# Optimization experiments

Hardware: AMD Instinct MI355X
Metric: run time of the kernel (lower is better)

The kernel has to match this reference:

```python
import jax, jax.numpy as jnp
import numpy as np

A, L, D_ATOM, D_PROT, B = 2048, 512, 128, 128, 64
H1, H2 = 512, 256


def setup_inputs() -> dict:
    key = jax.random.key(0)
    ks = jax.random.split(key, 10)
    atom_embed = jax.random.normal(ks[0], (A, D_ATOM), dtype=jnp.float32)
    protSeq_embed = jax.random.normal(ks[1], (B, L, D_PROT), dtype=jnp.float32)
    atom_splits = jnp.sort(jax.random.randint(ks[2], (A,), 0, B))
    # attention bilinear weight (atom_dim, prot_dim); scaled so exp(score) stays finite
    W_att = jax.random.normal(ks[3], (D_ATOM, D_PROT), dtype=jnp.float32) / np.float32(D_ATOM)
    cdim = D_ATOM + D_PROT
    W1 = jax.random.normal(ks[4], (cdim, H1), dtype=jnp.float32) / np.sqrt(np.float32(cdim))
    b1 = jnp.zeros((H1,), dtype=jnp.float32)
    W2 = jax.random.normal(ks[5], (H1, H2), dtype=jnp.float32) / np.sqrt(np.float32(H1))
    b2 = jnp.zeros((H2,), dtype=jnp.float32)
    Wo = jax.random.normal(ks[6], (H2, 1), dtype=jnp.float32) / np.sqrt(np.float32(H2))
    bo = jnp.zeros((1,), dtype=jnp.float32)
    return {"atom_embed": atom_embed, "protSeq_embed": protSeq_embed,
            "atom_splits": atom_splits, "W_att": W_att,
            "W1": W1, "b1": b1, "W2": W2, "b2": b2, "Wo": Wo, "bo": bo}


def reference(atom_embed, protSeq_embed, atom_splits, W_att, W1, b1, W2, b2, Wo, bo):
    batch = protSeq_embed.shape[0]
    # bilinear attention scores: S[a, l] = atom[a] @ W_att @ prot[seg[a], l]
    X = atom_embed @ W_att                              # [A, D_PROT]
    prot_g = protSeq_embed[atom_splits]                 # [A, L, D_PROT] (gather)
    S = jnp.einsum('ad,ald->al', X, prot_g)             # [A, L]
    # segment softmax over atoms within each molecule (on max-over-protein score)
    Wc = jnp.exp(jnp.max(S, axis=-1, keepdims=True))    # [A, 1]
    Sc = jax.ops.segment_sum(Wc, atom_splits, num_segments=batch)[atom_splits]
    aa = Wc / Sc                                        # [A, 1]
    atom_pool = jax.ops.segment_sum(aa * atom_embed, atom_splits, num_segments=batch)  # [B, D_ATOM]
    # protein attention: segment-max pooled scores -> softmax over residues
    Wp = jax.ops.segment_max(S, atom_splits, num_segments=batch)  # [B, L]
    ap = jax.nn.softmax(Wp, axis=-1)
    prot_pool = jnp.einsum('bl,bld->bd', ap, protSeq_embed)       # [B, D_PROT]
    h = jnp.concatenate([atom_pool, prot_pool], axis=-1)
    h = jax.nn.relu(h @ W1 + b1)
    h = jax.nn.relu(h @ W2 + b2)
    return h @ Wo + bo                                  # [B, 1]
```

## Files before the change

### kernel.cpp

```cpp
#include <hip/hip_runtime.h>
#include <math.h>

#define A_N 2048
#define L_N 512
#define D 128
#define B_N 64
#define H1_N 512
#define H2_N 256
#define NCHUNK 8
#define CL 64
#define XT 32
#define PST 136

typedef __attribute__((ext_vector_type(8))) short short8;
typedef __attribute__((ext_vector_type(4))) float f32x4;

__device__ __forceinline__ int lb_dev(const int* __restrict__ arr, int n, int val) {
    int lo = 0, hi = n;
    while (lo < hi) { int mid = (lo + hi) >> 1; if (arr[mid] < val) lo = mid + 1; else hi = mid; }
    return lo;
}

__device__ __forceinline__ float blk_sum(float v, float* red, int tid) {
    #pragma unroll
    for (int off = 32; off >= 1; off >>= 1) v += __shfl_xor(v, off);
    __syncthreads();
    if ((tid & 63) == 0) red[tid >> 6] = v;
    __syncthreads();
    return red[0] + red[1] + red[2] + red[3];
}

__device__ __forceinline__ unsigned short f2bf(float f) {
    unsigned int u = __float_as_uint(f);
    return (unsigned short)((u + 0x7FFFu + ((u >> 16) & 1u)) >> 16);
}
__device__ __forceinline__ float bf2f(unsigned short h) {
    return __uint_as_float(((unsigned int)h) << 16);
}

__global__ __launch_bounds__(256) void k1_xmul(const float* __restrict__ atom_embed,
                                               const float* __restrict__ W_att,
                                               const float* __restrict__ bo,
                                               float* __restrict__ X,
                                               float* __restrict__ out) {
    __shared__ float ae[8][128];
    const int tid = threadIdx.x;
    const int bid = blockIdx.x;
    if (bid == 0 && tid < B_N) out[tid] = bo[0];
    const int a0 = bid * 8;
    float4 v = reinterpret_cast<const float4*>(atom_embed + (size_t)a0 * D)[tid];
    const int fi = tid * 4;
    *reinterpret_cast<float4*>(&ae[fi >> 7][fi & 127]) = v;
    __syncthreads();
    const int d = tid & 127;
    const int ai = tid >> 7;
    float acc0 = 0.f, acc1 = 0.f, acc2 = 0.f, acc3 = 0.f;
    for (int k = 0; k < D; ++k) {
        const float w = W_att[k * D + d];
        acc0 += ae[ai + 0][k] * w;
        acc1 += ae[ai + 2][k] * w;
        acc2 += ae[ai + 4][k] * w;
        acc3 += ae[ai + 6][k] * w;
    }
    X[(size_t)(a0 + ai + 0) * D + d] = acc0;
    X[(size_t)(a0 + ai + 2) * D + d] = acc1;
    X[(size_t)(a0 + ai + 4) * D + d] = acc2;
    X[(size_t)(a0 + ai + 6) * D + d] = acc3;
}

__global__ __launch_bounds__(256) void k2_scores(const float* __restrict__ X,
                                                 const float* __restrict__ prot,
                                                 const int* __restrict__ splits,
                                                 float* __restrict__ rowmaxp,
                                                 float* __restrict__ ppart,
                                                 float* __restrict__ eWpart) {
    __shared__ __align__(16) unsigned char lds[52736];
    unsigned short* Ph = (unsigned short*)lds;
    unsigned short* Pl = Ph + CL * PST;
    unsigned short* Xh = Pl + CL * PST;
    unsigned short* Xl = Xh + XT * PST;
    float* rm_lds = (float*)(lds + 52224);

    const int tid = threadIdx.x;
    const int bid = blockIdx.x;
    const int b = bid & (B_N - 1);
    const int chunk = bid >> 6;
    const int l0 = chunk * CL;
    const int s = lb_dev(splits, A_N, b);
    const int e = lb_dev(splits, A_N, b + 1);
    const int n = e - s;
    const int lane = tid & 63;
    const int w = tid >> 6;
    const int col = lane & 15;
    const int kb = lane >> 4;

    {
        const float4* src = (const float4*)(prot + ((size_t)b * L_N + l0) * D);
        for (int i = tid; i < CL * (D / 4); i += 256) {
            float4 v = src[i];
            const int row = i >> 5, q = (i & 31) * 4;
            ushort4 h, lo;
            h.x = f2bf(v.x); lo.x = f2bf(v.x - bf2f(h.x));
            h.y = f2bf(v.y); lo.y = f2bf(v.y - bf2f(h.y));
            h.z = f2bf(v.z); lo.z = f2bf(v.z - bf2f(h.z));
            h.w = f2bf(v.w); lo.w = f2bf(v.w - bf2f(h.w));
            *(ushort4*)(Ph + row * PST + q) = h;
            *(ushort4*)(Pl + row * PST + q) = lo;
        }
    }
    __syncthreads();

    short8 Bh[4], Bl[4];
    {
        const int rowb = w * 16 + col;
        #pragma unroll
        for (int ks = 0; ks < 4; ++ks) {
            Bh[ks] = *(const short8*)(Ph + rowb * PST + ks * 32 + kb * 8);
            Bl[ks] = *(const short8*)(Pl + rowb * PST + ks * 32 + kb * 8);
        }
    }

    float cmrun = -INFINITY;
    for (int a0 = 0; a0 < n; a0 += XT) {
        __syncthreads();
        {
            const float4* xsrc = (const float4*)(X + (size_t)s * D);
            for (int i = tid; i < XT * (D / 4); i += 256) {
                const int row = i >> 5, q = (i & 31) * 4;
                const int atom = a0 + row;
                float4 v = {0.f, 0.f, 0.f, 0.f};
                if (atom < n) v = xsrc[(size_t)atom * (D / 4) + (i & 31)];
                ushort4 h, lo;
                h.x = f2bf(v.x); lo.x = f2bf(v.x - bf2f(h.x));
                h.y = f2bf(v.y); lo.y = f2bf(v.y - bf2f(h.y));
                h.z = f2bf(v.z); lo.z = f2bf(v.z - bf2f(h.z));
                h.w = f2bf(v.w); lo.w = f2bf(v.w - bf2f(h.w));
                *(ushort4*)(Xh + row * PST + q) = h;
                *(ushort4*)(Xl + row * PST + q) = lo;
            }
        }
        __syncthreads();

        #pragma unroll
        for (int mt = 0; mt < 2; ++mt) {
            f32x4 acc = {0.f, 0.f, 0.f, 0.f};
            const int rowa = mt * 16 + col;
            #pragma unroll
            for (int ks = 0; ks < 4; ++ks) {
                short8 Ah = *(const short8*)(Xh + rowa * PST + ks * 32 + kb * 8);
                short8 Al = *(const short8*)(Xl + rowa * PST + ks * 32 + kb * 8);
                acc = __builtin_amdgcn_mfma_f32_16x16x32_bf16(Ah, Bh[ks], acc, 0, 0, 0);
                acc = __builtin_amdgcn_mfma_f32_16x16x32_bf16(Ah, Bl[ks], acc, 0, 0, 0);
                acc = __builtin_amdgcn_mfma_f32_16x16x32_bf16(Al, Bh[ks], acc, 0, 0, 0);
            }
            float r0 = acc[0], r1 = acc[1], r2 = acc[2], r3 = acc[3];
            #pragma unroll
            for (int off = 1; off <= 8; off <<= 1) {
                r0 = fmaxf(r0, __shfl_xor(r0, off));
                r1 = fmaxf(r1, __shfl_xor(r1, off));
                r2 = fmaxf(r2, __shfl_xor(r2, off));
                r3 = fmaxf(r3, __shfl_xor(r3, off));
            }
            if (col == 0) {
                float4 rv; rv.x = r0; rv.y = r1; rv.z = r2; rv.w = r3;
                *(float4*)(rm_lds + w * 32 + mt * 16 + kb * 4) = rv;
            }
            const int rbase = a0 + mt * 16 + kb * 4;
            float cm = -INFINITY;
            if (rbase + 0 < n) cm = fmaxf(cm, acc[0]);
            if (rbase + 1 < n) cm = fmaxf(cm, acc[1]);
            if (rbase + 2 < n) cm = fmaxf(cm, acc[2]);
            if (rbase + 3 < n) cm = fmaxf(cm, acc[3]);
            cm = fmaxf(cm, __shfl_xor(cm, 16));
            cm = fmaxf(cm, __shfl_xor(cm, 32));
            cmrun = fmaxf(cmrun, cm);
        }
        __syncthreads();
        if (tid < XT) {
            const int atom = a0 + tid;
            if (atom < n) {
                float m = fmaxf(fmaxf(rm_lds[tid], rm_lds[32 + tid]),
                                fmaxf(rm_lds[64 + tid], rm_lds[96 + tid]));
                rowmaxp[(size_t)(s + atom) * NCHUNK + chunk] = m;
            }
        }
    }

    float* ews  = (float*)(lds + 34816);
    float* psum = ews + 64;
    __syncthreads();
    if (lane < 16) ews[w * 16 + lane] = expf(cmrun);
    __syncthreads();
    {
        const int dd = tid & 127, hh = tid >> 7;
        float sacc = 0.f;
        #pragma unroll 8
        for (int l = hh * 32; l < hh * 32 + 32; ++l)
            sacc += ews[l] * (bf2f(Ph[l * PST + dd]) + bf2f(Pl[l * PST + dd]));
        psum[hh * 128 + dd] = sacc;
    }
    __syncthreads();
    if (tid < 128)
        ppart[(size_t)(b * NCHUNK + chunk) * D + tid] = psum[tid] + psum[128 + tid];
    if (tid < 64) {
        float v = ews[tid];
        #pragma unroll
        for (int off = 32; off >= 1; off >>= 1) v += __shfl_xor(v, off);
        if (tid == 0) eWpart[b * NCHUNK + chunk] = v;
    }
}

__global__ __launch_bounds__(256) void k3_pool(const float* __restrict__ atom_embed,
                                               const int* __restrict__ splits,
                                               const float* __restrict__ rowmaxp,
                                               const float* __restrict__ ppart,
                                               const float* __restrict__ eWpart,
                                               float* __restrict__ HcT) {
    __shared__ float red[4];
    __shared__ float coef[512];
    __shared__ float4 pred[8][32];
    const int tid = threadIdx.x;
    const int b = blockIdx.x;
    const int s = lb_dev(splits, A_N, b);
    const int e = lb_dev(splits, A_N, b + 1);
    const int n = e - s;

    float local = 0.f;
    for (int j = tid; j < n; j += 256) {
        const float* rp = rowmaxp + (size_t)(s + j) * NCHUNK;
        float m = rp[0];
        #pragma unroll
        for (int c = 1; c < NCHUNK; ++c) m = fmaxf(m, rp[c]);
        local += expf(m);
    }
    const float Sc = blk_sum(local, red, tid);

    const int d4 = tid & 31;
    const int ag = tid >> 5;
    const float4* ae4 = reinterpret_cast<const float4*>(atom_embed);
    float4 pool = {0.f, 0.f, 0.f, 0.f};
    for (int t0 = 0; t0 < n; t0 += 512) {
        const int cnt = min(512, n - t0);
        __syncthreads();
        for (int j = tid; j < cnt; j += 256) {
            const float* rp = rowmaxp + (size_t)(s + t0 + j) * NCHUNK;
            float m = rp[0];
            #pragma unroll
            for (int c = 1; c < NCHUNK; ++c) m = fmaxf(m, rp[c]);
            coef[j] = expf(m) / Sc;
        }
        __syncthreads();
        for (int j = ag; j < cnt; j += 8) {
            const float c = coef[j];
            const float4 v = ae4[(size_t)(s + t0 + j) * (D / 4) + d4];
            pool.x += c * v.x; pool.y += c * v.y; pool.z += c * v.z; pool.w += c * v.w;
        }
    }
    __syncthreads();
    pred[ag][d4] = pool;
    __syncthreads();
    if (ag == 0) {
        float4 acc = pred[0][d4];
        #pragma unroll
        for (int gg = 1; gg < 8; ++gg) {
            const float4 t = pred[gg][d4];
            acc.x += t.x; acc.y += t.y; acc.z += t.z; acc.w += t.w;
        }
        HcT[(size_t)(d4 * 4 + 0) * B_N + b] = acc.x;
        HcT[(size_t)(d4 * 4 + 1) * B_N + b] = acc.y;
        HcT[(size_t)(d4 * 4 + 2) * B_N + b] = acc.z;
        HcT[(size_t)(d4 * 4 + 3) * B_N + b] = acc.w;
    }
    if (tid < 128) {
        float v = 0.f, ez = 0.f;
        #pragma unroll
        for (int c = 0; c < NCHUNK; ++c) {
            v  += ppart[(size_t)(b * NCHUNK + c) * D + tid];
            ez += eWpart[b * NCHUNK + c];
        }
        HcT[(size_t)(D + tid) * B_N + b] = v / ez;
    }
}

__global__ __launch_bounds__(256) void k4_h1(const float* __restrict__ HcT,
                                             const float* __restrict__ W1,
                                             const float* __restrict__ b1,
                                             float* __restrict__ H1T) {
    __shared__ float hr[4][64];
    const int tid = threadIdx.x;
    const int m = tid & 63;
    const int jh = (tid >> 6) & 1;
    const int kh = tid >> 7;
    const int j = blockIdx.x * 2 + jh;
    float acc = 0.f;
    const int k0 = kh * 128;
    #pragma unroll 8
    for (int k = k0; k < k0 + 128; ++k)
        acc += HcT[(size_t)k * B_N + m] * W1[(size_t)k * H1_N + j];
    hr[jh * 2 + kh][m] = acc;
    __syncthreads();
    if (kh == 0)
        H1T[(size_t)j * B_N + m] = fmaxf(hr[jh * 2][m] + hr[jh * 2 + 1][m] + b1[j], 0.f);
}

__global__ __launch_bounds__(256) void k5_h2(const float* __restrict__ H1T,
                                             const float* __restrict__ W2,
                                             const float* __restrict__ b2,
                                             const float* __restrict__ Wo,
                                             float* __restrict__ out) {
    __shared__ float hr[4][64];
    const int tid = threadIdx.x;
    const int m = tid & 63;
    const int kq = tid >> 6;
    const int j = blockIdx.x;
    float acc = 0.f;
    const int k0 = kq * 128;
    #pragma unroll 8
    for (int k = k0; k < k0 + 128; ++k)
        acc += H1T[(size_t)k * B_N + m] * W2[(size_t)k * H2_N + j];
    hr[kq][m] = acc;
    __syncthreads();
    if (kq == 0) {
        const float h2 = fmaxf(hr[0][m] + hr[1][m] + hr[2][m] + hr[3][m] + b2[j], 0.f);
        atomicAdd(out + m, h2 * Wo[j]);
    }
}

extern "C" void kernel_launch(void* const* d_in, const int* in_sizes, int n_in,
                              void* d_out, int out_size, void* d_ws, size_t ws_size,
                              hipStream_t stream) {
    const float* atom_embed = (const float*)d_in[0];
    const float* prot       = (const float*)d_in[1];
    const int*   splits     = (const int*)d_in[2];
    const float* W_att      = (const float*)d_in[3];
    const float* W1         = (const float*)d_in[4];
    const float* b1         = (const float*)d_in[5];
    const float* W2         = (const float*)d_in[6];
    const float* b2         = (const float*)d_in[7];
    const float* Wo         = (const float*)d_in[8];
    const float* bo         = (const float*)d_in[9];
    float* out = (float*)d_out;

    float* ws = (float*)d_ws;
    float* X       = ws;  ws += A_N * D;
    float* rowmaxp = ws;  ws += A_N * NCHUNK;
    float* ppart   = ws;  ws += B_N * NCHUNK * D;
    float* eWpart  = ws;  ws += B_N * NCHUNK;
    float* HcT     = ws;  ws += 2 * D * B_N;
    float* H1T     = ws;  ws += H1_N * B_N;

    hipLaunchKernelGGL(k1_xmul,  dim3(A_N / 8),      dim3(256), 0, stream,
                       atom_embed, W_att, bo, X, out);
    hipLaunchKernelGGL(k2_scores,dim3(B_N * NCHUNK), dim3(256), 0, stream,
                       X, prot, splits, rowmaxp, ppart, eWpart);
    hipLaunchKernelGGL(k3_pool,  dim3(B_N),          dim3(256), 0, stream,
                       atom_embed, splits, rowmaxp, ppart, eWpart, HcT);
    hipLaunchKernelGGL(k4_h1,    dim3(H1_N / 2),     dim3(256), 0, stream, HcT, W1, b1, H1T);
    hipLaunchKernelGGL(k5_h2,    dim3(H2_N),         dim3(256), 0, stream, H1T, W2, b2, Wo, out);
}
```

Before: 46.23 us.

## Fuse projection, scoring and pooling into one per-molecule kernel

Merges the X=atom@W_att projection (now done with split-bf16 MFMA in-block), the score computation and both pooling stages into one kernel with one block per molecule. This removes the X, rowmax and partial-sum workspace round trips and two kernel launches. In exchange the grid shrinks from 512 blocks to 64, and each block streams the full protein sequence once per 64-atom tile while recomputing W_att fragments from global memory. That lowers parallelism and may leave most CUs idle.

Result: slower. 64.28 us (+39.0%).

```diff
diff --git a/kernel.cpp b/kernel.cpp
--- a/kernel.cpp
+++ b/kernel.cpp
@@ -7,9 +7,6 @@
 #define B_N 64
 #define H1_N 512
 #define H2_N 256
-#define NCHUNK 8
-#define CL 64
-#define XT 32
 #define PST 136
 
 typedef __attribute__((ext_vector_type(8))) short short8;
@@ -21,15 +18,6 @@
     return lo;
 }
 
-__device__ __forceinline__ float blk_sum(float v, float* red, int tid) {
-    #pragma unroll
-    for (int off = 32; off >= 1; off >>= 1) v += __shfl_xor(v, off);
-    __syncthreads();
-    if ((tid & 63) == 0) red[tid >> 6] = v;
-    __syncthreads();
-    return red[0] + red[1] + red[2] + red[3];
-}
-
 __device__ __forceinline__ unsigned short f2bf(float f) {
     unsigned int u = __float_as_uint(f);
     return (unsigned short)((u + 0x7FFFu + ((u >> 16) & 1u)) >> 16);
@@ -38,247 +26,274 @@
     return __uint_as_float(((unsigned int)h) << 16);
 }
 
-__global__ __launch_bounds__(256) void k1_xmul(const float* __restrict__ atom_embed,
-                                               const float* __restrict__ W_att,
-                                               const float* __restrict__ bo,
-                                               float* __restrict__ X,
-                                               float* __restrict__ out) {
-    __shared__ float ae[8][128];
+__global__ __launch_bounds__(256) void k123(const float* __restrict__ atom_embed,
+                                            const float* __restrict__ prot,
+                                            const int* __restrict__ splits,
+                                            const float* __restrict__ W_att,
+                                            const float* __restrict__ bo,
+                                            float* __restrict__ HcT,
+                                            float* __restrict__ out) {
+    __shared__ unsigned short Ph[32 * PST], Pl[32 * PST];
+    __shared__ unsigned short Xh[64 * PST], Xl[64 * PST];
+    __shared__ float cmax_all[512];
+    __shared__ float rm[64];
+    __shared__ float rm_part[4][64];
+    __shared__ float cm_part[2][32];
+    __shared__ float ews[32];
+    __shared__ float ea_lds[64];
+    __shared__ float4 pred[8][32];
+    __shared__ float zacc_s, sc_acc_s;
+
     const int tid = threadIdx.x;
-    const int bid = blockIdx.x;
-    if (bid == 0 && tid < B_N) out[tid] = bo[0];
-    const int a0 = bid * 8;
-    float4 v = reinterpret_cast<const float4*>(atom_embed + (size_t)a0 * D)[tid];
-    const int fi = tid * 4;
-    *reinterpret_cast<float4*>(&ae[fi >> 7][fi & 127]) = v;
-    __syncthreads();
-    const int d = tid & 127;
-    const int ai = tid >> 7;
-    float acc0 = 0.f, acc1 = 0.f, acc2 = 0.f, acc3 = 0.f;
-    for (int k = 0; k < D; ++k) {
-        const float w = W_att[k * D + d];
-        acc0 += ae[ai + 0][k] * w;
-        acc1 += ae[ai + 2][k] * w;
-        acc2 += ae[ai + 4][k] * w;
-        acc3 += ae[ai + 6][k] * w;
-    }
-    X[(size_t)(a0 + ai + 0) * D + d] = acc0;
-    X[(size_t)(a0 + ai + 2) * D + d] = acc1;
-    X[(size_t)(a0 + ai + 4) * D + d] = acc2;
-    X[(size_t)(a0 + ai + 6) * D + d] = acc3;
-}
-
-__global__ __launch_bounds__(256) void k2_scores(const float* __restrict__ X,
-                                                 const float* __restrict__ prot,
-                                                 const int* __restrict__ splits,
-                                                 float* __restrict__ rowmaxp,
-                                                 float* __restrict__ ppart,
-                                                 float* __restrict__ eWpart) {
-    __shared__ __align__(16) unsigned char lds[52736];
-    unsigned short* Ph = (unsigned short*)lds;
-    unsigned short* Pl = Ph + CL * PST;
-    unsigned short* Xh = Pl + CL * PST;
-    unsigned short* Xl = Xh + XT * PST;
-    float* rm_lds = (float*)(lds + 52224);
-
-    const int tid = threadIdx.x;
-    const int bid = blockIdx.x;
-    const int b = bid & (B_N - 1);
-    const int chunk = bid >> 6;
-    const int l0 = chunk * CL;
+    const int b = blockIdx.x;
+    if (b == 0 && tid < B_N) out[tid] = bo[0];
     const int s = lb_dev(splits, A_N, b);
     const int e = lb_dev(splits, A_N, b + 1);
     const int n = e - s;
+
+    cmax_all[tid] = -INFINITY;
+    cmax_all[tid + 256] = -INFINITY;
+    if (tid < 64) rm[tid] = -INFINITY;
+    if (tid == 0) { zacc_s = 0.f; sc_acc_s = 0.f; }
+
     const int lane = tid & 63;
     const int w = tid >> 6;
     const int col = lane & 15;
     const int kb = lane >> 4;
-
-    {
-        const float4* src = (const float4*)(prot + ((size_t)b * L_N + l0) * D);
-        for (int i = tid; i < CL * (D / 4); i += 256) {
-            float4 v = src[i];
-            const int row = i >> 5, q = (i & 31) * 4;
-            ushort4 h, lo;
-            h.x = f2bf(v.x); lo.x = f2bf(v.x - bf2f(h.x));
-            h.y = f2bf(v.y); lo.y = f2bf(v.y - bf2f(h.y));
-            h.z = f2bf(v.z); lo.z = f2bf(v.z - bf2f(h.z));
-            h.w = f2bf(v.w); lo.w = f2bf(v.w - bf2f(h.w));
-            *(ushort4*)(Ph + row * PST + q) = h;
-            *(ushort4*)(Pl + row * PST + q) = lo;
-        }
-    }
-    __syncthreads();
-
-    short8 Bh[4], Bl[4];
-    {
-        const int rowb = w * 16 + col;
-        #pragma unroll
-        for (int ks = 0; ks < 4; ++ks) {
-            Bh[ks] = *(const short8*)(Ph + rowb * PST + ks * 32 + kb * 8);
-            Bl[ks] = *(const short8*)(Pl + rowb * PST + ks * 32 + kb * 8);
-        }
-    }
-
-    float cmrun = -INFINITY;
-    for (int a0 = 0; a0 < n; a0 += XT) {
+    const int c4 = tid & 31;
+    const int rg = tid >> 5;
+
+    float4 pool4 = {0.f, 0.f, 0.f, 0.f};
+    float4 pp4   = {0.f, 0.f, 0.f, 0.f};
+
+    for (int a0 = 0; a0 < n; a0 += 64) {
+        const int an = min(64, n - a0);
+        const bool isLast = (a0 + 64 >= n);
+
         __syncthreads();
         {
-            const float4* xsrc = (const float4*)(X + (size_t)s * D);
-            for (int i = tid; i < XT * (D / 4); i += 256) {
-                const int row = i >> 5, q = (i & 31) * 4;
-                const int atom = a0 + row;
-                float4 v = {0.f, 0.f, 0.f, 0.f};
-                if (atom < n) v = xsrc[(size_t)atom * (D / 4) + (i & 31)];
-                ushort4 h, lo;
-                h.x = f2bf(v.x); lo.x = f2bf(v.x - bf2f(h.x));
-                h.y = f2bf(v.y); lo.y = f2bf(v.y - bf2f(h.y));
-                h.z = f2bf(v.z); lo.z = f2bf(v.z - bf2f(h.z));
-                h.w = f2bf(v.w); lo.w = f2bf(v.w - bf2f(h.w));
-                *(ushort4*)(Xh + row * PST + q) = h;
-                *(ushort4*)(Xl + row * PST + q) = lo;
+            short8 WBh[2][4], WBl[2][4];
+            #pragma unroll
+            for (int ff = 0; ff < 2; ++ff) {
+                const int dcol = (w * 2 + ff) * 16 + col;
+                #pragma unroll
+                for (int ks = 0; ks < 4; ++ks) {
+                    short8 bh, bl;
+                    #pragma unroll
+                    for (int j = 0; j < 8; ++j) {
+                        const float wv = W_att[(size_t)(ks * 32 + kb * 8 + j) * D + dcol];
+                        const unsigned short h = f2bf(wv);
+                        bh[j] = (short)h;
+                        bl[j] = (short)f2bf(wv - bf2f(h));
+                    }
+                    WBh[ff][ks] = bh; WBl[ff][ks] = bl;
+                }
+            }
+            #pragma unroll
+            for (int mt = 0; mt < 4; ++mt) {
+                const int ar = mt * 16 + col;
+                const bool va = ar < an;
+                short8 Ah[4], Al[4];
+                #pragma unroll
+                for (int ks = 0; ks < 4; ++ks) {
+                    float4 v0 = {0.f,0.f,0.f,0.f}, v1 = {0.f,0.f,0.f,0.f};
+                    if (va) {
+                        const float4* p = (const float4*)(atom_embed + (size_t)(s + a0 + ar) * D)
+                                          + ks * 8 + kb * 2;
+                        v0 = p[0]; v1 = p[1];
+                    }
+                    const float vv[8] = {v0.x,v0.y,v0.z,v0.w,v1.x,v1.y,v1.z,v1.w};
+                    short8 ah, al;
+                    #pragma unroll
+                    for (int j = 0; j < 8; ++j) {
+                        const unsigned short h = f2bf(vv[j]);
+                        ah[j] = (short)h;
+                        al[j] = (short)f2bf(vv[j] - bf2f(h));
+                    }
+                    Ah[ks] = ah; Al[ks] = al;
+                }
+                #pragma unroll
+                for (int ff = 0; ff < 2; ++ff) {
+                    f32x4 acc = {0.f, 0.f, 0.f, 0.f};
+                    #pragma unroll
+                    for (int ks = 0; ks < 4; ++ks) {
+                        acc = __builtin_amdgcn_mfma_f32_16x16x32_bf16(Ah[ks], WBh[ff][ks], acc, 0, 0, 0);
+                        acc = __builtin_amdgcn_mfma_f32_16x16x32_bf16(Ah[ks], WBl[ff][ks], acc, 0, 0, 0);
+                        acc = __builtin_amdgcn_mfma_f32_16x16x32_bf16(Al[ks], WBh[ff][ks], acc, 0, 0, 0);
+                    }
+                    const int dcol = (w * 2 + ff) * 16 + col;
+                    #pragma unroll
+                    for (int i = 0; i < 4; ++i) {
+                        const int arow = mt * 16 + kb * 4 + i;
+                        const unsigned short h = f2bf(acc[i]);
+                        Xh[arow * PST + dcol] = h;
+                        Xl[arow * PST + dcol] = f2bf(acc[i] - bf2f(h));
+                    }
+                }
             }
         }
         __syncthreads();
 
+        short8 XAh[2][4], XAl[2][4];
         #pragma unroll
-        for (int mt = 0; mt < 2; ++mt) {
-            f32x4 acc = {0.f, 0.f, 0.f, 0.f};
-            const int rowa = mt * 16 + col;
+        for (int m = 0; m < 2; ++m) {
+            const int mrow = ((w >> 1) + m * 2) * 16 + col;
             #pragma unroll
             for (int ks = 0; ks < 4; ++ks) {
-                short8 Ah = *(const short8*)(Xh + rowa * PST + ks * 32 + kb * 8);
-                short8 Al = *(const short8*)(Xl + rowa * PST + ks * 32 + kb * 8);
-                acc = __builtin_amdgcn_mfma_f32_16x16x32_bf16(Ah, Bh[ks], acc, 0, 0, 0);
-                acc = __builtin_amdgcn_mfma_f32_16x16x32_bf16(Ah, Bl[ks], acc, 0, 0, 0);
-                acc = __builtin_amdgcn_mfma_f32_16x16x32_bf16(Al, Bh[ks], acc, 0, 0, 0);
-            }
-            float r0 = acc[0], r1 = acc[1], r2 = acc[2], r3 = acc[3];
-            #pragma unroll
-            for (int off = 1; off <= 8; off <<= 1) {
-                r0 = fmaxf(r0, __shfl_xor(r0, off));
-                r1 = fmaxf(r1, __shfl_xor(r1, off));
-                r2 = fmaxf(r2, __shfl_xor(r2, off));
-                r3 = fmaxf(r3, __shfl_xor(r3, off));
-            }
-            if (col == 0) {
-                float4 rv; rv.x = r0; rv.y = r1; rv.z = r2; rv.w = r3;
-                *(float4*)(rm_lds + w * 32 + mt * 16 + kb * 4) = rv;
-            }
-            const int rbase = a0 + mt * 16 + kb * 4;
-            float cm = -INFINITY;
-            if (rbase + 0 < n) cm = fmaxf(cm, acc[0]);
-            if (rbase + 1 < n) cm = fmaxf(cm, acc[1]);
-            if (rbase + 2 < n) cm = fmaxf(cm, acc[2]);
-            if (rbase + 3 < n) cm = fmaxf(cm, acc[3]);
-            cm = fmaxf(cm, __shfl_xor(cm, 16));
-            cm = fmaxf(cm, __shfl_xor(cm, 32));
-            cmrun = fmaxf(cmrun, cm);
+                XAh[m][ks] = *(const short8*)(Xh + mrow * PST + ks * 32 + kb * 8);
+                XAl[m][ks] = *(const short8*)(Xl + mrow * PST + ks * 32 + kb * 8);
+            }
+        }
+
+        for (int ch = 0; ch < 16; ++ch) {
+            __syncthreads();
+            float4 pv[4];
+            {
+                const float4* src = (const float4*)(prot + ((size_t)b * L_N + ch * 32) * D);
+                #pragma unroll
+                for (int kq = 0; kq < 4; ++kq) {
+                    const int i = tid + kq * 256;
+                    pv[kq] = src[i];
+                    const int row = i >> 5, q = (i & 31) * 4;
+                    ushort4 h, lo;
+                    h.x = f2bf(pv[kq].x); lo.x = f2bf(pv[kq].x - bf2f(h.x));
+                    h.y = f2bf(pv[kq].y); lo.y = f2bf(pv[kq].y - bf2f(h.y));
+                    h.z = f2bf(pv[kq].z); lo.z = f2bf(pv[kq].z - bf2f(h.z));
+                    h.w = f2bf(pv[kq].w); lo.w = f2bf(pv[kq].w - bf2f(h.w));
+                    *(ushort4*)(Ph + row * PST + q) = h;
+                    *(ushort4*)(Pl + row * PST + q) = lo;
+                }
+            }
+            ((float*)rm_part)[tid] = -INFINITY;
+            __syncthreads();
+
+            const int nt = w & 1;
+            short8 PBh[4], PBl[4];
+            #pragma unroll
+            for (int ks = 0; ks < 4; ++ks) {
+                PBh[ks] = *(const short8*)(Ph + (nt * 16 + col) * PST + ks * 32 + kb * 8);
+                PBl[ks] = *(const short8*)(Pl + (nt * 16 + col) * PST + ks * 32 + kb * 8);
+            }
+            float cm_w = -INFINITY;
+            #pragma unroll
+            for (int m = 0; m < 2; ++m) {
+                f32x4 acc = {0.f, 0.f, 0.f, 0.f};
+                #pragma unroll
+                for (int ks = 0; ks < 4; ++ks) {
+                    acc = __builtin_amdgcn_mfma_f32_16x16x32_bf16(XAh[m][ks], PBh[ks], acc, 0, 0, 0);
+                    acc = __builtin_amdgcn_mfma_f32_16x16x32_bf16(XAh[m][ks], PBl[ks], acc, 0, 0, 0);
+                    acc = __builtin_amdgcn_mfma_f32_16x16x32_bf16(XAl[m][ks], PBh[ks], acc, 0, 0, 0);
+                }
+                const int mt = (w >> 1) + m * 2;
+                float r0 = acc[0], r1 = acc[1], r2 = acc[2], r3 = acc[3];
+                #pragma unroll
+                for (int off = 1; off <= 8; off <<= 1) {
+                    r0 = fmaxf(r0, __shfl_xor(r0, off));
+                    r1 = fmaxf(r1, __shfl_xor(r1, off));
+                    r2 = fmaxf(r2, __shfl_xor(r2, off));
+                    r3 = fmaxf(r3, __shfl_xor(r3, off));
+                }
+                if (col == 0) {
+                    rm_part[w][mt * 16 + kb * 4 + 0] = r0;
+                    rm_part[w][mt * 16 + kb * 4 + 1] = r1;
+                    rm_part[w][mt * 16 + kb * 4 + 2] = r2;
+                    rm_part[w][mt * 16 + kb * 4 + 3] = r3;
+                }
+                const int rb = mt * 16 + kb * 4;
+                float cm = -INFINITY;
+                if (rb + 0 < an) cm = fmaxf(cm, acc[0]);
+                if (rb + 1 < an) cm = fmaxf(cm, acc[1]);
+                if (rb + 2 < an) cm = fmaxf(cm, acc[2]);
+                if (rb + 3 < an) cm = fmaxf(cm, acc[3]);
+                cm = fmaxf(cm, __shfl_xor(cm, 16));
+                cm = fmaxf(cm, __shfl_xor(cm, 32));
+                cm_w = fmaxf(cm_w, cm);
+            }
+            if (kb == 0) cm_part[w >> 1][nt * 16 + col] = cm_w;
+            __syncthreads();
+
+            if (tid < 64) {
+                const float m4 = fmaxf(fmaxf(rm_part[0][tid], rm_part[1][tid]),
+                                       fmaxf(rm_part[2][tid], rm_part[3][tid]));
+                rm[tid] = fmaxf(rm[tid], m4);
+            }
+            if (tid < 32) {
+                const float cm = fmaxf(cm_part[0][tid], cm_part[1][tid]);
+                const float cl = fmaxf(cmax_all[ch * 32 + tid], cm);
+                cmax_all[ch * 32 + tid] = cl;
+                if (isLast) {
+                    float ev = expf(cl);
+                    ews[tid] = ev;
+                    #pragma unroll
+                    for (int off = 1; off <= 16; off <<= 1) ev += __shfl_xor(ev, off);
+                    if (tid == 0) zacc_s += ev;
+                }
+            }
+            __syncthreads();
+
+            if (isLast) {
+                #pragma unroll
+                for (int kq = 0; kq < 4; ++kq) {
+                    const float wgt = ews[rg + kq * 8];
+                    pp4.x += wgt * pv[kq].x;
+                    pp4.y += wgt * pv[kq].y;
+                    pp4.z += wgt * pv[kq].z;
+                    pp4.w += wgt * pv[kq].w;
+                }
+            }
+        }
+
+        if (tid < 64) {
+            float ea = (tid < an) ? expf(rm[tid]) : 0.f;
+            ea_lds[tid] = ea;
+            rm[tid] = -INFINITY;
+            #pragma unroll
+            for (int off = 1; off <= 32; off <<= 1) ea += __shfl_xor(ea, off);
+            if (tid == 0) sc_acc_s += ea;
         }
         __syncthreads();
-        if (tid < XT) {
-            const int atom = a0 + tid;
-            if (atom < n) {
-                float m = fmaxf(fmaxf(rm_lds[tid], rm_lds[32 + tid]),
-                                fmaxf(rm_lds[64 + tid], rm_lds[96 + tid]));
-                rowmaxp[(size_t)(s + atom) * NCHUNK + chunk] = m;
+        {
+            const float4* ae4 = (const float4*)atom_embed;
+            for (int a = rg; a < an; a += 8) {
+                const float c = ea_lds[a];
+                const float4 v = ae4[(size_t)(s + a0 + a) * (D / 4) + c4];
+                pool4.x += c * v.x; pool4.y += c * v.y;
+                pool4.z += c * v.z; pool4.w += c * v.w;
             }
         }
     }
 
-    float* ews  = (float*)(lds + 34816);
-    float* psum = ews + 64;
-    __syncthreads();
-    if (lane < 16) ews[w * 16 + lane] = expf(cmrun);
-    __syncthreads();
-    {
-        const int dd = tid & 127, hh = tid >> 7;
-        float sacc = 0.f;
-        #pragma unroll 8
-        for (int l = hh * 32; l < hh * 32 + 32; ++l)
-            sacc += ews[l] * (bf2f(Ph[l * PST + dd]) + bf2f(Pl[l * PST + dd]));
-        psum[hh * 128 + dd] = sacc;
-    }
-    __syncthreads();
-    if (tid < 128)
-        ppart[(size_t)(b * NCHUNK + chunk) * D + tid] = psum[tid] + psum[128 + tid];
-    if (tid < 64) {
-        float v = ews[tid];
-        #pragma unroll
-        for (int off = 32; off >= 1; off >>= 1) v += __shfl_xor(v, off);
-        if (tid == 0) eWpart[b * NCHUNK + chunk] = v;
-    }
-}
-
-__global__ __launch_bounds__(256) void k3_pool(const float* __restrict__ atom_embed,
-                                               const int* __restrict__ splits,
-                                               const float* __restrict__ rowmaxp,
-                                               const float* __restrict__ ppart,
-                                               const float* __restrict__ eWpart,
-                                               float* __restrict__ HcT) {
-    __shared__ float red[4];
-    __shared__ float coef[512];
-    __shared__ float4 pred[8][32];
-    const int tid = threadIdx.x;
-    const int b = blockIdx.x;
-    const int s = lb_dev(splits, A_N, b);
-    const int e = lb_dev(splits, A_N, b + 1);
-    const int n = e - s;
-
-    float local = 0.f;
-    for (int j = tid; j < n; j += 256) {
-        const float* rp = rowmaxp + (size_t)(s + j) * NCHUNK;
-        float m = rp[0];
-        #pragma unroll
-        for (int c = 1; c < NCHUNK; ++c) m = fmaxf(m, rp[c]);
-        local += expf(m);
-    }
-    const float Sc = blk_sum(local, red, tid);
-
-    const int d4 = tid & 31;
-    const int ag = tid >> 5;
-    const float4* ae4 = reinterpret_cast<const float4*>(atom_embed);
-    float4 pool = {0.f, 0.f, 0.f, 0.f};
-    for (int t0 = 0; t0 < n; t0 += 512) {
-        const int cnt = min(512, n - t0);
-        __syncthreads();
-        for (int j = tid; j < cnt; j += 256) {
-            const float* rp = rowmaxp + (size_t)(s + t0 + j) * NCHUNK;
-            float m = rp[0];
-            #pragma unroll
-            for (int c = 1; c < NCHUNK; ++c) m = fmaxf(m, rp[c]);
-            coef[j] = expf(m) / Sc;
-        }
-        __syncthreads();
-        for (int j = ag; j < cnt; j += 8) {
-            const float c = coef[j];
-            const float4 v = ae4[(size_t)(s + t0 + j) * (D / 4) + d4];
-            pool.x += c * v.x; pool.y += c * v.y; pool.z += c * v.z; pool.w += c * v.w;
-        }
-    }
-    __syncthreads();
-    pred[ag][d4] = pool;
-    __syncthreads();
-    if (ag == 0) {
-        float4 acc = pred[0][d4];
+    __syncthreads();
+    pred[rg][c4] = pool4;
+    __syncthreads();
+    if (tid < 32) {
+        float4 acc = pred[0][tid];
         #pragma unroll
         for (int gg = 1; gg < 8; ++gg) {
-            const float4 t = pred[gg][d4];
+            const float4 t = pred[gg][tid];
             acc.x += t.x; acc.y += t.y; acc.z += t.z; acc.w += t.w;
         }
-        HcT[(size_t)(d4 * 4 + 0) * B_N + b] = acc.x;
-        HcT[(size_t)(d4 * 4 + 1) * B_N + b] = acc.y;
-        HcT[(size_t)(d4 * 4 + 2) * B_N + b] = acc.z;
-        HcT[(size_t)(d4 * 4 + 3) * B_N + b] = acc.w;
+        const float invSc = 1.f / sc_acc_s;
+        HcT[(size_t)(tid * 4 + 0) * B_N + b] = acc.x * invSc;
+        HcT[(size_t)(tid * 4 + 1) * B_N + b] = acc.y * invSc;
+        HcT[(size_t)(tid * 4 + 2) * B_N + b] = acc.z * invSc;
+        HcT[(size_t)(tid * 4 + 3) * B_N + b] = acc.w * invSc;
     }
-    if (tid < 128) {
-        float v = 0.f, ez = 0.f;
+    __syncthreads();
+    pred[rg][c4] = pp4;
+    __syncthreads();
+    if (tid < 32) {
+        float4 acc = pred[0][tid];
         #pragma unroll
-        for (int c = 0; c < NCHUNK; ++c) {
-            v  += ppart[(size_t)(b * NCHUNK + c) * D + tid];
-            ez += eWpart[b * NCHUNK + c];
-        }
-        HcT[(size_t)(D + tid) * B_N + b] = v / ez;
+        for (int gg = 1; gg < 8; ++gg) {
+            const float4 t = pred[gg][tid];
+            acc.x += t.x; acc.y += t.y; acc.z += t.z; acc.w += t.w;
+        }
+        const float invZ = 1.f / zacc_s;
+        HcT[(size_t)(D + tid * 4 + 0) * B_N + b] = acc.x * invZ;
+        HcT[(size_t)(D + tid * 4 + 1) * B_N + b] = acc.y * invZ;
+        HcT[(size_t)(D + tid * 4 + 2) * B_N + b] = acc.z * invZ;
+        HcT[(size_t)(D + tid * 4 + 3) * B_N + b] = acc.w * invZ;
     }
 }
 
@@ -342,19 +357,11 @@
     float* out = (float*)d_out;
 
     float* ws = (float*)d_ws;
-    float* X       = ws;  ws += A_N * D;
-    float* rowmaxp = ws;  ws += A_N * NCHUNK;
-    float* ppart   = ws;  ws += B_N * NCHUNK * D;
-    float* eWpart  = ws;  ws += B_N * NCHUNK;
-    float* HcT     = ws;  ws += 2 * D * B_N;
-    float* H1T     = ws;  ws += H1_N * B_N;
-
-    hipLaunchKernelGGL(k1_xmul,  dim3(A_N / 8),      dim3(256), 0, stream,
-                       atom_embed, W_att, bo, X, out);
-    hipLaunchKernelGGL(k2_scores,dim3(B_N * NCHUNK), dim3(256), 0, stream,
-                       X, prot, splits, rowmaxp, ppart, eWpart);
-    hipLaunchKernelGGL(k3_pool,  dim3(B_N),          dim3(256), 0, stream,
-                       atom_embed, splits, rowmaxp, ppart, eWpart, HcT);
-    hipLaunchKernelGGL(k4_h1,    dim3(H1_N / 2),     dim3(256), 0, stream, HcT, W1, b1, H1T);
-    hipLaunchKernelGGL(k5_h2,    dim3(H2_N),         dim3(256), 0, stream, H1T, W2, b2, Wo, out);
-}
+    float* HcT = ws;  ws += 2 * D * B_N;
+    float* H1T = ws;  ws += H1_N * B_N;
+
+    hipLaunchKernelGGL(k123, dim3(B_N),      dim3(256), 0, stream,
+                       atom_embed, prot, splits, W_att, bo, HcT, out);
+    hipLaunchKernelGGL(k4_h1, dim3(H1_N / 2), dim3(256), 0, stream, HcT, W1, b1, H1T);
+    hipLaunchKernelGGL(k5_h2, dim3(H2_N),     dim3(256), 0, stream, H1T, W2, b2, Wo, out);
+}
```

## Precompute bf16 hi/lo X in k1 and drop LDS staging in scores kernel

Applied to the files above, without the earlier changes.

k1 now writes X already split into bf16 high and low halves, so k2 no longer converts X on every chunk. The scores kernel drops its LDS tiles for X and prot: each wave loads its B fragments straight from global memory and streams A fragments per 16-atom tile. Chunks shrink to 32 residues, doubling the grid to 1024 blocks, and a launch bound asks for 3 blocks per CU. The weighted protein sum now rereads fp32 prot from global memory instead of LDS. The per-block row-max buffer holds only 128 atoms per molecule, so larger segments would overflow it.

Result: slower. 49.66 us (+7.4%).

```diff
diff --git a/kernel.cpp b/kernel.cpp
--- a/kernel.cpp
+++ b/kernel.cpp
@@ -7,10 +7,8 @@
 #define B_N 64
 #define H1_N 512
 #define H2_N 256
-#define NCHUNK 8
-#define CL 64
-#define XT 32
-#define PST 136
+#define NCHUNK 16
+#define CL 32
 
 typedef __attribute__((ext_vector_type(8))) short short8;
 typedef __attribute__((ext_vector_type(4))) float f32x4;
@@ -41,7 +39,8 @@
 __global__ __launch_bounds__(256) void k1_xmul(const float* __restrict__ atom_embed,
                                                const float* __restrict__ W_att,
                                                const float* __restrict__ bo,
-                                               float* __restrict__ X,
+                                               unsigned short* __restrict__ Xh,
+                                               unsigned short* __restrict__ Xl,
                                                float* __restrict__ out) {
     __shared__ float ae[8][128];
     const int tid = threadIdx.x;
@@ -62,24 +61,27 @@
         acc2 += ae[ai + 4][k] * w;
         acc3 += ae[ai + 6][k] * w;
     }
-    X[(size_t)(a0 + ai + 0) * D + d] = acc0;
-    X[(size_t)(a0 + ai + 2) * D + d] = acc1;
-    X[(size_t)(a0 + ai + 4) * D + d] = acc2;
-    X[(size_t)(a0 + ai + 6) * D + d] = acc3;
-}
-
-__global__ __launch_bounds__(256) void k2_scores(const float* __restrict__ X,
-                                                 const float* __restrict__ prot,
-                                                 const int* __restrict__ splits,
-                                                 float* __restrict__ rowmaxp,
-                                                 float* __restrict__ ppart,
-                                                 float* __restrict__ eWpart) {
-    __shared__ __align__(16) unsigned char lds[52736];
-    unsigned short* Ph = (unsigned short*)lds;
-    unsigned short* Pl = Ph + CL * PST;
-    unsigned short* Xh = Pl + CL * PST;
-    unsigned short* Xl = Xh + XT * PST;
-    float* rm_lds = (float*)(lds + 52224);
+    float accs[4] = {acc0, acc1, acc2, acc3};
+    #pragma unroll
+    for (int t = 0; t < 4; ++t) {
+        const size_t idx = (size_t)(a0 + ai + 2 * t) * D + d;
+        const unsigned short h = f2bf(accs[t]);
+        Xh[idx] = h;
+        Xl[idx] = f2bf(accs[t] - bf2f(h));
+    }
+}
+
+__global__ __launch_bounds__(256, 3) void k2_scores(const unsigned short* __restrict__ Xh,
+                                                    const unsigned short* __restrict__ Xl,
+                                                    const float* __restrict__ prot,
+                                                    const int* __restrict__ splits,
+                                                    float* __restrict__ rowmaxp,
+                                                    float* __restrict__ ppart,
+                                                    float* __restrict__ eWpart) {
+    __shared__ float rm_part[2][128];
+    __shared__ float cm_part[2][32];
+    __shared__ float ews_s[CL];
+    __shared__ float4 pred[8][32];
 
     const int tid = threadIdx.x;
     const int bid = blockIdx.x;
@@ -89,124 +91,125 @@
     const int s = lb_dev(splits, A_N, b);
     const int e = lb_dev(splits, A_N, b + 1);
     const int n = e - s;
+
     const int lane = tid & 63;
     const int w = tid >> 6;
     const int col = lane & 15;
     const int kb = lane >> 4;
-
-    {
-        const float4* src = (const float4*)(prot + ((size_t)b * L_N + l0) * D);
-        for (int i = tid; i < CL * (D / 4); i += 256) {
-            float4 v = src[i];
-            const int row = i >> 5, q = (i & 31) * 4;
-            ushort4 h, lo;
-            h.x = f2bf(v.x); lo.x = f2bf(v.x - bf2f(h.x));
-            h.y = f2bf(v.y); lo.y = f2bf(v.y - bf2f(h.y));
-            h.z = f2bf(v.z); lo.z = f2bf(v.z - bf2f(h.z));
-            h.w = f2bf(v.w); lo.w = f2bf(v.w - bf2f(h.w));
-            *(ushort4*)(Ph + row * PST + q) = h;
-            *(ushort4*)(Pl + row * PST + q) = lo;
-        }
-    }
+    const int lt = w & 1;
+    const int pair = w >> 1;
+
+    ((float*)rm_part)[tid] = -INFINITY;
+    if (tid < 64) ((float*)cm_part)[tid] = -INFINITY;
     __syncthreads();
 
     short8 Bh[4], Bl[4];
     {
-        const int rowb = w * 16 + col;
+        const float4* pb = (const float4*)(prot + ((size_t)(b * L_N + l0 + lt * 16 + col)) * D);
         #pragma unroll
         for (int ks = 0; ks < 4; ++ks) {
-            Bh[ks] = *(const short8*)(Ph + rowb * PST + ks * 32 + kb * 8);
-            Bl[ks] = *(const short8*)(Pl + rowb * PST + ks * 32 + kb * 8);
+            const float4 v0 = pb[ks * 8 + kb * 2];
+            const float4 v1 = pb[ks * 8 + kb * 2 + 1];
+            const float vv[8] = {v0.x, v0.y, v0.z, v0.w, v1.x, v1.y, v1.z, v1.w};
+            short8 bh, bl;
+            #pragma unroll
+            for (int j = 0; j < 8; ++j) {
+                const unsigned short h = f2bf(vv[j]);
+                bh[j] = (short)h;
+                bl[j] = (short)f2bf(vv[j] - bf2f(h));
+            }
+            Bh[ks] = bh; Bl[ks] = bl;
         }
     }
 
     float cmrun = -INFINITY;
-    for (int a0 = 0; a0 < n; a0 += XT) {
-        __syncthreads();
-        {
-            const float4* xsrc = (const float4*)(X + (size_t)s * D);
-            for (int i = tid; i < XT * (D / 4); i += 256) {
-                const int row = i >> 5, q = (i & 31) * 4;
-                const int atom = a0 + row;
-                float4 v = {0.f, 0.f, 0.f, 0.f};
-                if (atom < n) v = xsrc[(size_t)atom * (D / 4) + (i & 31)];
-                ushort4 h, lo;
-                h.x = f2bf(v.x); lo.x = f2bf(v.x - bf2f(h.x));
-                h.y = f2bf(v.y); lo.y = f2bf(v.y - bf2f(h.y));
-                h.z = f2bf(v.z); lo.z = f2bf(v.z - bf2f(h.z));
-                h.w = f2bf(v.w); lo.w = f2bf(v.w - bf2f(h.w));
-                *(ushort4*)(Xh + row * PST + q) = h;
-                *(ushort4*)(Xl + row * PST + q) = lo;
-            }
-        }
-        __syncthreads();
-
-        #pragma unroll
-        for (int mt = 0; mt < 2; ++mt) {
-            f32x4 acc = {0.f, 0.f, 0.f, 0.f};
-            const int rowa = mt * 16 + col;
-            #pragma unroll
-            for (int ks = 0; ks < 4; ++ks) {
-                short8 Ah = *(const short8*)(Xh + rowa * PST + ks * 32 + kb * 8);
-                short8 Al = *(const short8*)(Xl + rowa * PST + ks * 32 + kb * 8);
-                acc = __builtin_amdgcn_mfma_f32_16x16x32_bf16(Ah, Bh[ks], acc, 0, 0, 0);
-                acc = __builtin_amdgcn_mfma_f32_16x16x32_bf16(Ah, Bl[ks], acc, 0, 0, 0);
-                acc = __builtin_amdgcn_mfma_f32_16x16x32_bf16(Al, Bh[ks], acc, 0, 0, 0);
-            }
-            float r0 = acc[0], r1 = acc[1], r2 = acc[2], r3 = acc[3];
-            #pragma unroll
-            for (int off = 1; off <= 8; off <<= 1) {
-                r0 = fmaxf(r0, __shfl_xor(r0, off));
-                r1 = fmaxf(r1, __shfl_xor(r1, off));
-                r2 = fmaxf(r2, __shfl_xor(r2, off));
-                r3 = fmaxf(r3, __shfl_xor(r3, off));
-            }
-            if (col == 0) {
-                float4 rv; rv.x = r0; rv.y = r1; rv.z = r2; rv.w = r3;
-                *(float4*)(rm_lds + w * 32 + mt * 16 + kb * 4) = rv;
-            }
-            const int rbase = a0 + mt * 16 + kb * 4;
-            float cm = -INFINITY;
-            if (rbase + 0 < n) cm = fmaxf(cm, acc[0]);
-            if (rbase + 1 < n) cm = fmaxf(cm, acc[1]);
-            if (rbase + 2 < n) cm = fmaxf(cm, acc[2]);
-            if (rbase + 3 < n) cm = fmaxf(cm, acc[3]);
-            cm = fmaxf(cm, __shfl_xor(cm, 16));
-            cm = fmaxf(cm, __shfl_xor(cm, 32));
-            cmrun = fmaxf(cmrun, cm);
-        }
-        __syncthreads();
-        if (tid < XT) {
-            const int atom = a0 + tid;
-            if (atom < n) {
-                float m = fmaxf(fmaxf(rm_lds[tid], rm_lds[32 + tid]),
-                                fmaxf(rm_lds[64 + tid], rm_lds[96 + tid]));
-                rowmaxp[(size_t)(s + atom) * NCHUNK + chunk] = m;
-            }
-        }
-    }
-
-    float* ews  = (float*)(lds + 34816);
-    float* psum = ews + 64;
-    __syncthreads();
-    if (lane < 16) ews[w * 16 + lane] = expf(cmrun);
-    __syncthreads();
-    {
-        const int dd = tid & 127, hh = tid >> 7;
-        float sacc = 0.f;
-        #pragma unroll 8
-        for (int l = hh * 32; l < hh * 32 + 32; ++l)
-            sacc += ews[l] * (bf2f(Ph[l * PST + dd]) + bf2f(Pl[l * PST + dd]));
-        psum[hh * 128 + dd] = sacc;
-    }
-    __syncthreads();
-    if (tid < 128)
-        ppart[(size_t)(b * NCHUNK + chunk) * D + tid] = psum[tid] + psum[128 + tid];
-    if (tid < 64) {
-        float v = ews[tid];
-        #pragma unroll
-        for (int off = 32; off >= 1; off >>= 1) v += __shfl_xor(v, off);
+    for (int at = pair; at * 16 < n; at += 2) {
+        const int arow = min(s + at * 16 + col, A_N - 1);
+        const unsigned short* xh = Xh + (size_t)arow * D;
+        const unsigned short* xl = Xl + (size_t)arow * D;
+        short8 Ah[4], Al[4];
+        #pragma unroll
+        for (int ks = 0; ks < 4; ++ks) {
+            Ah[ks] = *(const short8*)(xh + ks * 32 + kb * 8);
+            Al[ks] = *(const short8*)(xl + ks * 32 + kb * 8);
+        }
+        f32x4 aHH = {0.f, 0.f, 0.f, 0.f};
+        f32x4 aHL = {0.f, 0.f, 0.f, 0.f};
+        f32x4 aLH = {0.f, 0.f, 0.f, 0.f};
+        #pragma unroll
+        for (int ks = 0; ks < 4; ++ks) {
+            aHH = __builtin_amdgcn_mfma_f32_16x16x32_bf16(Ah[ks], Bh[ks], aHH, 0, 0, 0);
+            aHL = __builtin_amdgcn_mfma_f32_16x16x32_bf16(Ah[ks], Bl[ks], aHL, 0, 0, 0);
+            aLH = __builtin_amdgcn_mfma_f32_16x16x32_bf16(Al[ks], Bh[ks], aLH, 0, 0, 0);
+        }
+        float r[4];
+        #pragma unroll
+        for (int i = 0; i < 4; ++i) r[i] = aHH[i] + aHL[i] + aLH[i];
+
+        float r0 = r[0], r1 = r[1], r2 = r[2], r3 = r[3];
+        #pragma unroll
+        for (int off = 1; off <= 8; off <<= 1) {
+            r0 = fmaxf(r0, __shfl_xor(r0, off));
+            r1 = fmaxf(r1, __shfl_xor(r1, off));
+            r2 = fmaxf(r2, __shfl_xor(r2, off));
+            r3 = fmaxf(r3, __shfl_xor(r3, off));
+        }
+        if (col == 0) {
+            rm_part[lt][at * 16 + kb * 4 + 0] = r0;
+            rm_part[lt][at * 16 + kb * 4 + 1] = r1;
+            rm_part[lt][at * 16 + kb * 4 + 2] = r2;
+            rm_part[lt][at * 16 + kb * 4 + 3] = r3;
+        }
+        const int rb = at * 16 + kb * 4;
+        float cm = -INFINITY;
+        if (rb + 0 < n) cm = fmaxf(cm, r[0]);
+        if (rb + 1 < n) cm = fmaxf(cm, r[1]);
+        if (rb + 2 < n) cm = fmaxf(cm, r[2]);
+        if (rb + 3 < n) cm = fmaxf(cm, r[3]);
+        cm = fmaxf(cm, __shfl_xor(cm, 16));
+        cm = fmaxf(cm, __shfl_xor(cm, 32));
+        cmrun = fmaxf(cmrun, cm);
+    }
+    if (kb == 0) cm_part[pair][lt * 16 + col] = cmrun;
+    __syncthreads();
+
+    if (tid < 128 && tid < n)
+        rowmaxp[(size_t)(s + tid) * NCHUNK + chunk] = fmaxf(rm_part[0][tid], rm_part[1][tid]);
+    if (tid >= 128 && tid < 128 + CL) {
+        const int l = tid - 128;
+        ews_s[l] = expf(fmaxf(cm_part[0][l], cm_part[1][l]));
+    }
+    __syncthreads();
+
+    if (tid < 32) {
+        float v = ews_s[tid];
+        #pragma unroll
+        for (int off = 1; off <= 16; off <<= 1) v += __shfl_xor(v, off);
         if (tid == 0) eWpart[b * NCHUNK + chunk] = v;
+    }
+
+    const int rg = tid >> 5, c4 = tid & 31;
+    float4 pp4 = {0.f, 0.f, 0.f, 0.f};
+    const float4* src = (const float4*)(prot + ((size_t)b * L_N + l0) * D);
+    #pragma unroll
+    for (int q = 0; q < 4; ++q) {
+        const int i = tid + q * 256;
+        const float4 v = src[i];
+        const float wgt = ews_s[i >> 5];
+        pp4.x += wgt * v.x; pp4.y += wgt * v.y;
+        pp4.z += wgt * v.z; pp4.w += wgt * v.w;
+    }
+    pred[rg][c4] = pp4;
+    __syncthreads();
+    if (tid < 32) {
+        float4 acc = pred[0][tid];
+        #pragma unroll
+        for (int gg = 1; gg < 8; ++gg) {
+            const float4 t = pred[gg][tid];
+            acc.x += t.x; acc.y += t.y; acc.z += t.z; acc.w += t.w;
+        }
+        float* dst = ppart + (size_t)(b * NCHUNK + chunk) * D + tid * 4;
+        dst[0] = acc.x; dst[1] = acc.y; dst[2] = acc.z; dst[3] = acc.w;
     }
 }
 
@@ -341,20 +344,21 @@
     const float* bo         = (const float*)d_in[9];
     float* out = (float*)d_out;
 
-    float* ws = (float*)d_ws;
-    float* X       = ws;  ws += A_N * D;
-    float* rowmaxp = ws;  ws += A_N * NCHUNK;
-    float* ppart   = ws;  ws += B_N * NCHUNK * D;
-    float* eWpart  = ws;  ws += B_N * NCHUNK;
-    float* HcT     = ws;  ws += 2 * D * B_N;
-    float* H1T     = ws;  ws += H1_N * B_N;
-
-    hipLaunchKernelGGL(k1_xmul,  dim3(A_N / 8),      dim3(256), 0, stream,
-                       atom_embed, W_att, bo, X, out);
-    hipLaunchKernelGGL(k2_scores,dim3(B_N * NCHUNK), dim3(256), 0, stream,
-                       X, prot, splits, rowmaxp, ppart, eWpart);
-    hipLaunchKernelGGL(k3_pool,  dim3(B_N),          dim3(256), 0, stream,
+    unsigned short* Xh = (unsigned short*)d_ws;
+    unsigned short* Xl = Xh + (size_t)A_N * D;
+    float* fp      = (float*)(Xl + (size_t)A_N * D);
+    float* rowmaxp = fp;  fp += (size_t)A_N * NCHUNK;
+    float* ppart   = fp;  fp += (size_t)B_N * NCHUNK * D;
+    float* eWpart  = fp;  fp += B_N * NCHUNK;
+    float* HcT     = fp;  fp += 2 * D * B_N;
+    float* H1T     = fp;  fp += H1_N * B_N;
+
+    hipLaunchKernelGGL(k1_xmul,  dim3(A_N / 8),        dim3(256), 0, stream,
+                       atom_embed, W_att, bo, Xh, Xl, out);
+    hipLaunchKernelGGL(k2_scores, dim3(B_N * NCHUNK),  dim3(256), 0, stream,
+                       Xh, Xl, prot, splits, rowmaxp, ppart, eWpart);
+    hipLaunchKernelGGL(k3_pool,  dim3(B_N),            dim3(256), 0, stream,
                        atom_embed, splits, rowmaxp, ppart, eWpart, HcT);
-    hipLaunchKernelGGL(k4_h1,    dim3(H1_N / 2),     dim3(256), 0, stream, HcT, W1, b1, H1T);
-    hipLaunchKernelGGL(k5_h2,    dim3(H2_N),         dim3(256), 0, stream, H1T, W2, b2, Wo, out);
-}
+    hipLaunchKernelGGL(k4_h1,    dim3(H1_N / 2),       dim3(256), 0, stream, HcT, W1, b1, H1T);
+    hipLaunchKernelGGL(k5_h2,    dim3(H2_N),           dim3(256), 0, stream, H1T, W2, b2, Wo, out);
+}
```
